# Kernel optimization log

Hardware: AMD Instinct MI355X
Metric: run time of the kernel (lower is better)

## Reference

```python
import jax, jax.numpy as jnp
import numpy as np

GAMMA = 10.0                      # self.gamma
MU = jnp.arange(0.0, 2.0, 0.1)    # self.mu_k, D=20
ORDER = 2                         # order arg to Stream


def setup_inputs() -> dict:
    key = jax.random.key(0)
    ks = jax.random.split(key, 6)
    B, N, F, D, Fv = 8, 512, 16, 20, 1
    coordinates = jax.random.uniform(ks[0], (B, N, 3), dtype=jnp.float32)
    atom_emb = jax.random.normal(ks[1], (1, 1, Fv), dtype=jnp.float32)   # xavier-style atom embedding
    W_e = jax.random.normal(ks[2], (D, F), dtype=jnp.float32) / np.sqrt(D)
    b_e = jnp.zeros((F,), jnp.float32)
    w_a = jax.random.normal(ks[3], (F,), dtype=jnp.float32) / np.sqrt(F)
    Wq = jax.random.normal(ks[4], (Fv, 1), dtype=jnp.float32)            # Q: Linear(F_v -> 1)
    bq = jnp.zeros((1,), jnp.float32)
    return dict(coordinates=coordinates, atom_emb=atom_emb, W_e=W_e,
                b_e=b_e, w_a=w_a, Wq=Wq, bq=bq)


def reference(coordinates, atom_emb, W_e, b_e, w_a, Wq, bq):
    B, N, _ = coordinates.shape
    # adjacency: pairwise Euclidean distances (B,N,N)
    diff = coordinates[:, :, None, :] - coordinates[:, None, :, :]
    d = jnp.sqrt(jnp.sum(diff * diff, axis=-1) + 1e-12)
    # rbf_expansion: Gaussian basis; original materializes (B,N,N,D) broadcasts
    rbf_d = jnp.exp(-GAMMA * (d[..., None] - MU) ** 2)   # (B,N,N,D)
    rbf_0 = jnp.exp(-GAMMA * MU ** 2)                    # (D,) basis at d=0 (constant over pairs)
    # geometric attention stream: edge features from RBF -> scalar attention
    feat_d = jnp.tanh(jnp.einsum('bnmd,df->bnmf', rbf_d, W_e) + b_e)  # (B,N,N,F)
    feat_0 = jnp.tanh(rbf_0 @ W_e + b_e)                              # (F,)
    # subtracting the d=0 baseline zeroes self-interaction on the diagonal
    alpha = jnp.einsum('bnmf,f->bnm', feat_d, w_a) - jnp.dot(feat_0, w_a)
    # message passing of order-k correlations over atom embeddings
    v = jnp.broadcast_to(atom_emb, (B, N, atom_emb.shape[-1]))  # (B,N,F_v)
    for _ in range(ORDER):
        v = v + jnp.einsum('bnm,bmf->bnf', alpha, v) / N
    # take stream output for node 0 and project: v_[:, 0, :] -> Q(.)
    return v[:, 0, :] @ Wq + bq  # (B,1)
```

## Files before the change

kernel.cpp:

```cpp
#include <hip/hip_runtime.h>
#include <math.h>


#define BB 8
#define NN 512
#define FF 16
#define DD 20
#define TBL 2048
#define DMAX 1.7320509f

#define WS_PART_OFF TBL
#define WS_S0_OFF (TBL + 512)

__device__ __forceinline__ float eval_g(float d, const float* __restrict__ We,
                                        const float* __restrict__ be,
                                        const float* __restrict__ wa) {
    float z[FF];
#pragma unroll
    for (int f = 0; f < FF; ++f) z[f] = be[f];
#pragma unroll
    for (int k = 0; k < DD; ++k) {
        float u = d - 0.1f * (float)k;
        float r = __expf(-10.0f * u * u);
#pragma unroll
        for (int f = 0; f < FF; ++f) z[f] = fmaf(r, We[k * FF + f], z[f]);
    }
    float g = 0.0f;
#pragma unroll
    for (int f = 0; f < FF; ++f) g += wa[f] * tanhf(z[f]);
    return g;
}

__global__ __launch_bounds__(256) void build_table(const float* __restrict__ We,
                                                   const float* __restrict__ be,
                                                   const float* __restrict__ wa,
                                                   float* __restrict__ ws) {
    int i = blockIdx.x * blockDim.x + threadIdx.x;
    float d = (DMAX / (float)(TBL - 1)) * (float)i;
    ws[i] = eval_g(d, We, be, wa);
}

__global__ __launch_bounds__(256) void rows_partial(const float* __restrict__ coords,
                                                    float* __restrict__ ws) {
    __shared__ float sh[TBL];
    __shared__ float sc[NN * 3];
    __shared__ float wp[4][2];

    const int tid   = threadIdx.x;
    const int b     = blockIdx.x >> 5;
    const int chunk = blockIdx.x & 31;

    {
        const float4* lut4 = (const float4*)ws;
        float4* sh4 = (float4*)sh;
        sh4[tid]       = lut4[tid];
        sh4[tid + 256] = lut4[tid + 256];
        const float4* cb4 = (const float4*)(coords + (size_t)b * NN * 3);
        float4* sc4 = (float4*)sc;
        sc4[tid] = cb4[tid];
        if (tid < 128) sc4[tid + 256] = cb4[tid + 256];
    }
    __syncthreads();

    const int wave = tid >> 6;
    const int lane = tid & 63;
    const float inv_h = (float)(TBL - 1) / DMAX;
    const float g0 = sh[0];

    float p1 = 0.0f, p2 = 0.0f;
#pragma unroll
    for (int r = 0; r < 4; ++r) {
        const int n = chunk * 16 + wave * 4 + r;
        const float cx = sc[3 * n], cy = sc[3 * n + 1], cz = sc[3 * n + 2];
        float acc = 0.0f;
#pragma unroll
        for (int it = 0; it < 8; ++it) {
            const int m = lane + it * 64;
            float dx = cx - sc[3 * m];
            float dy = cy - sc[3 * m + 1];
            float dz = cz - sc[3 * m + 2];
            float dd = fmaf(dx, dx, fmaf(dy, dy, dz * dz)) + 1e-12f;
            float x  = sqrtf(dd) * inv_h;
            int  i0  = (int)x;
            i0 = (i0 < TBL - 2) ? i0 : (TBL - 2);
            float fr = x - (float)i0;
            float t0 = sh[i0], t1 = sh[i0 + 1];
            acc += fmaf(fr, t1 - t0, t0);
        }
#pragma unroll
        for (int off = 32; off > 0; off >>= 1) acc += __shfl_down(acc, off, 64);
        if (lane == 0) {
            float dx = sc[0] - cx, dy = sc[1] - cy, dz = sc[2] - cz;
            float dd = fmaf(dx, dx, fmaf(dy, dy, dz * dz)) + 1e-12f;
            float x  = sqrtf(dd) * inv_h;
            int  i0  = (int)x;
            i0 = (i0 < TBL - 2) ? i0 : (TBL - 2);
            float fr = x - (float)i0;
            float al = fmaf(fr, sh[i0 + 1] - sh[i0], sh[i0]) - g0;
            p1 += al;
            p2 += al * acc;
            if (chunk == 0 && n == 0) ws[WS_S0_OFF + b] = acc;
        }
    }
    if (lane == 0) { wp[wave][0] = p1; wp[wave][1] = p2; }
    __syncthreads();
    if (tid == 0) {
        float P1 = wp[0][0] + wp[1][0] + wp[2][0] + wp[3][0];
        float P2 = wp[0][1] + wp[1][1] + wp[2][1] + wp[3][1];
        ws[WS_PART_OFF + blockIdx.x * 2 + 0] = P1;
        ws[WS_PART_OFF + blockIdx.x * 2 + 1] = P2;
    }
}

__global__ __launch_bounds__(64) void finalize(const float* __restrict__ atom_emb,
                                               const float* __restrict__ Wq,
                                               const float* __restrict__ bq,
                                               const float* __restrict__ ws,
                                               float* __restrict__ out) {
    const int b = threadIdx.x;
    if (b < BB) {
        const float g0 = ws[0];
        const float a  = atom_emb[0];
        const float invN = 1.0f / (float)NN;
        float P1 = 0.0f, P2 = 0.0f;
        for (int j = 0; j < 32; ++j) {
            P1 += ws[WS_PART_OFF + (b * 32 + j) * 2 + 0];
            P2 += ws[WS_PART_OFF + (b * 32 + j) * 2 + 1];
        }
        float S0 = ws[WS_S0_OFF + b];
        float v1_0 = a * (1.0f + S0 * invN - g0);
        float corr = a * fmaf(P2, invN, (1.0f - g0) * P1);
        out[b] = fmaf(v1_0 + corr * invN, Wq[0], bq[0]);
    }
}

extern "C" void kernel_launch(void* const* d_in, const int* in_sizes, int n_in,
                              void* d_out, int out_size, void* d_ws, size_t ws_size,
                              hipStream_t stream) {
    const float* coords   = (const float*)d_in[0];
    const float* atom_emb = (const float*)d_in[1];
    const float* W_e      = (const float*)d_in[2];
    const float* b_e      = (const float*)d_in[3];
    const float* w_a      = (const float*)d_in[4];
    const float* Wq       = (const float*)d_in[5];
    const float* bq       = (const float*)d_in[6];
    float* out = (float*)d_out;
    float* ws  = (float*)d_ws;

    build_table<<<TBL / 256, 256, 0, stream>>>(W_e, b_e, w_a, ws);
    rows_partial<<<256, 256, 0, stream>>>(coords, ws);
    finalize<<<1, 64, 0, stream>>>(atom_emb, Wq, bq, ws, out);
}
```

Baseline: 82.88 us.

## Fuse lookup-table build into row kernel with smaller table and fast tanh

Removes the separate build_table launch. Each row block now computes its own 512-entry distance lookup table in shared memory, and finalize evaluates g(0) directly. The table shrinks from 2048 to 512 entries so every block can afford to build it, and tanhf is replaced by an exp/reciprocal approximation. This saves a kernel launch and a global round trip, at the cost of redundant table computation in all 256 blocks and coarser interpolation accuracy.

Measured after the change: 76.91 us. 1.08x faster.

```diff
diff --git a/kernel.cpp b/kernel.cpp
--- a/kernel.cpp
+++ b/kernel.cpp
@@ -6,11 +6,16 @@
 #define NN 512
 #define FF 16
 #define DD 20
-#define TBL 2048
+#define TBL 512
 #define DMAX 1.7320509f
 
-#define WS_PART_OFF TBL
-#define WS_S0_OFF (TBL + 512)
+#define WS_PART_OFF 0
+#define WS_S0_OFF 512
+
+__device__ __forceinline__ float fast_tanh(float x) {
+    float e = __expf(2.0f * x);
+    return 1.0f - 2.0f * __builtin_amdgcn_rcpf(e + 1.0f);
+}
 
 __device__ __forceinline__ float eval_g(float d, const float* __restrict__ We,
                                         const float* __restrict__ be,
@@ -27,20 +32,14 @@
     }
     float g = 0.0f;
 #pragma unroll
-    for (int f = 0; f < FF; ++f) g += wa[f] * tanhf(z[f]);
+    for (int f = 0; f < FF; ++f) g += wa[f] * fast_tanh(z[f]);
     return g;
 }
 
-__global__ __launch_bounds__(256) void build_table(const float* __restrict__ We,
-                                                   const float* __restrict__ be,
-                                                   const float* __restrict__ wa,
-                                                   float* __restrict__ ws) {
-    int i = blockIdx.x * blockDim.x + threadIdx.x;
-    float d = (DMAX / (float)(TBL - 1)) * (float)i;
-    ws[i] = eval_g(d, We, be, wa);
-}
-
 __global__ __launch_bounds__(256) void rows_partial(const float* __restrict__ coords,
+                                                    const float* __restrict__ We,
+                                                    const float* __restrict__ be,
+                                                    const float* __restrict__ wa,
                                                     float* __restrict__ ws) {
     __shared__ float sh[TBL];
     __shared__ float sc[NN * 3];
@@ -51,14 +50,13 @@
     const int chunk = blockIdx.x & 31;
 
     {
-        const float4* lut4 = (const float4*)ws;
-        float4* sh4 = (float4*)sh;
-        sh4[tid]       = lut4[tid];
-        sh4[tid + 256] = lut4[tid + 256];
         const float4* cb4 = (const float4*)(coords + (size_t)b * NN * 3);
         float4* sc4 = (float4*)sc;
         sc4[tid] = cb4[tid];
         if (tid < 128) sc4[tid + 256] = cb4[tid + 256];
+        const float h = DMAX / (float)(TBL - 1);
+        sh[tid]       = eval_g(h * (float)tid, We, be, wa);
+        sh[tid + 256] = eval_g(h * (float)(tid + 256), We, be, wa);
     }
     __syncthreads();
 
@@ -112,14 +110,17 @@
     }
 }
 
-__global__ __launch_bounds__(64) void finalize(const float* __restrict__ atom_emb,
+__global__ __launch_bounds__(64) void finalize(const float* __restrict__ We,
+                                               const float* __restrict__ be,
+                                               const float* __restrict__ wa,
+                                               const float* __restrict__ atom_emb,
                                                const float* __restrict__ Wq,
                                                const float* __restrict__ bq,
                                                const float* __restrict__ ws,
                                                float* __restrict__ out) {
     const int b = threadIdx.x;
     if (b < BB) {
-        const float g0 = ws[0];
+        const float g0 = eval_g(0.0f, We, be, wa);
         const float a  = atom_emb[0];
         const float invN = 1.0f / (float)NN;
         float P1 = 0.0f, P2 = 0.0f;
@@ -147,7 +148,6 @@
     float* out = (float*)d_out;
     float* ws  = (float*)d_ws;
 
-    build_table<<<TBL / 256, 256, 0, stream>>>(W_e, b_e, w_a, ws);
-    rows_partial<<<256, 256, 0, stream>>>(coords, ws);
-    finalize<<<1, 64, 0, stream>>>(atom_emb, Wq, bq, ws, out);
+    rows_partial<<<256, 256, 0, stream>>>(coords, W_e, b_e, w_a, ws);
+    finalize<<<1, 64, 0, stream>>>(W_e, b_e, w_a, atom_emb, Wq, bq, ws, out);
 }
```
